# Kernel optimization log

Measured on AMD Instinct MI355X. Metric: run time of the kernel, lower is better.

## Reference

```python
import jax, jax.numpy as jnp
import numpy as np

EMBED_DIM = 768
NUM_HEADS = 12
HEAD_DIM = EMBED_DIM // NUM_HEADS  # 64
SEGMENT_LENGTHS = (2048, 4096, 8192)
DILATION_RATES = (1, 2, 4)
LN_EPS = 1e-5


def setup_inputs() -> dict:
    key = jax.random.key(0)
    ks = jax.random.split(key, 8)
    B, N, E = 2, 8192, EMBED_DIM
    std = 1.0 / np.sqrt(E)
    return {
        "query": jax.random.normal(ks[0], (B, N, E), jnp.float32),
        "key": jax.random.normal(ks[1], (B, N, E), jnp.float32),
        "value": jax.random.normal(ks[2], (B, N, E), jnp.float32),
        "Wqkv": jax.random.normal(ks[3], (3 * E, E), jnp.float32) * std,
        "bqkv": jnp.zeros((3 * E,), jnp.float32),
        "Wo": jax.random.normal(ks[4], (E, E), jnp.float32) * std,
        "bo": jnp.zeros((E,), jnp.float32),
        "ln_w": jnp.ones((E,), jnp.float32),
        "ln_b": jnp.zeros((E,), jnp.float32),
        "is_causal": 0,
    }


def _dilated_attention(q, k, v, is_causal):
    # q, k, v: (b, n, h, d). Heads are partitioned into len(SEGMENT_LENGTHS) groups.
    b, n, h, d = q.shape
    ng = len(SEGMENT_LENGTHS)
    g = h // ng  # heads per group
    scale = 1.0 / np.sqrt(d)
    outs = []
    for i, (s, r) in enumerate(zip(SEGMENT_LENGTHS, DILATION_RATES)):
        off = i % r
        hs = slice(i * g, (i + 1) * g)
        m = n // s          # number of segments
        t = (s - off + r - 1) // r  # dilated tokens per segment
        # (b, m, s, g, d) -> dilated subsample -> (b, m, t, g, d)
        qi = q[:, :, hs].reshape(b, m, s, g, d)[:, :, off::r] * scale
        ki = k[:, :, hs].reshape(b, m, s, g, d)[:, :, off::r]
        vi = v[:, :, hs].reshape(b, m, s, g, d)[:, :, off::r]
        # attention within each segment over the dilated tokens
        scores = jnp.einsum("bmqhd,bmkhd->bmhqk", qi, ki)  # (b,m,g,t,t)
        if is_causal:
            mask = jnp.tril(jnp.ones((t, t), bool))
            scores = jnp.where(mask, scores, jnp.finfo(scores.dtype).min)
        attn = jax.nn.softmax(scores, axis=-1)
        xi = jnp.einsum("bmhqk,bmkhd->bmqhd", attn, vi)  # (b,m,t,g,d)
        # scatter back into full segment positions (zeros elsewhere)
        full = jnp.zeros((b, m, s, g, d), xi.dtype).at[:, :, off::r].set(xi)
        outs.append(full.reshape(b, n, g, d))
    return jnp.concatenate(outs, axis=2)  # (b, n, h, d)


def reference(query, key, value, Wqkv, bqkv, Wo, bo, ln_w, ln_b, is_causal):
    b, n, e = query.shape
    h, d = NUM_HEADS, HEAD_DIM
    q = (query @ Wqkv[:e].T + bqkv[:e]).reshape(b, n, h, d)
    k = (key @ Wqkv[e:2 * e].T + bqkv[e:2 * e]).reshape(b, n, h, d)
    v = (value @ Wqkv[2 * e:].T + bqkv[2 * e:]).reshape(b, n, h, d)
    x = _dilated_attention(q, k, v, is_causal).reshape(b, n, e)
    # LayerNorm
    mu = jnp.mean(x, axis=-1, keepdims=True)
    var = jnp.mean(jnp.square(x - mu), axis=-1, keepdims=True)
    x = (x - mu) * jax.lax.rsqrt(var + LN_EPS) * ln_w + ln_b
    return x @ Wo.T + bo
```

## Files before the change

### kernel.cpp

```cpp
#include <hip/hip_runtime.h>
#include <stdint.h>
#include <stddef.h>

typedef __bf16 bf16;
typedef __attribute__((ext_vector_type(4))) float f32x4;
typedef __attribute__((ext_vector_type(16))) float f32x16;
typedef __attribute__((ext_vector_type(8))) bf16 bf16x8;
typedef __attribute__((ext_vector_type(4))) bf16 bf16x4;

#define INST_STRIDE (2048 * 64)

static __device__ __forceinline__ f32x4 mfma16(bf16x8 a, bf16x8 b, f32x4 c) {
  return __builtin_amdgcn_mfma_f32_16x16x32_bf16(a, b, c, 0, 0, 0);
}
static __device__ __forceinline__ f32x16 mfma32(bf16x8 a, bf16x8 b, f32x16 c) {
  return __builtin_amdgcn_mfma_f32_32x32x16_bf16(a, b, c, 0, 0, 0);
}
static __device__ __forceinline__ void gload16(const void* g, void* l) {
  __builtin_amdgcn_global_load_lds(
      (const __attribute__((address_space(1))) void*)g,
      (__attribute__((address_space(3))) void*)l, 16, 0, 0);
}

__global__ void convert_w(const float* __restrict__ Wqkv, const float* __restrict__ Wo,
                          bf16* __restrict__ wq, bf16* __restrict__ wo) {
  int idx = blockIdx.x * 256 + threadIdx.x;
  const int NQ = 3 * 768 * 768 / 4;
  const float4* src;
  bf16* dst;
  int i;
  if (idx < NQ) { src = (const float4*)Wqkv; dst = wq; i = idx; }
  else          { src = (const float4*)Wo;   dst = wo; i = idx - NQ; }
  float4 v = src[i];
  bf16x4 o = { (bf16)v.x, (bf16)v.y, (bf16)v.z, (bf16)v.w };
  *(bf16x4*)(dst + (size_t)i * 4) = o;
}

__launch_bounds__(256, 4)
__global__ void qkv_gemm(const float* __restrict__ Xq, const float* __restrict__ Xk,
                         const float* __restrict__ Xv, const bf16* __restrict__ Wb,
                         const float* __restrict__ bqkv, bf16* __restrict__ qg,
                         bf16* __restrict__ kg, bf16* __restrict__ vtg) {
  __shared__ __align__(16) bf16 lA[128 * 64];
  __shared__ __align__(16) bf16 lB[128 * 64];
  const int z = blockIdx.z;
  const float* __restrict__ X = (z == 0) ? Xq : ((z == 1) ? Xk : Xv);
  const int bx = blockIdx.x;
  const int nt = blockIdx.y;
  int g, mt;
  if (bx < 128)      { g = 0; mt = bx; }
  else if (bx < 192) { g = 1; mt = bx - 128; }
  else               { g = 2; mt = bx - 192; }
  const int gshift = 13 - g;
  const int gpbm = (8192 >> g) - 1;
  const int ibase = (g == 2) ? 24 : (g << 4);
  const int nseg = 4 >> g;

  const int tid = threadIdx.x;
  const int lane = tid & 63, w = tid >> 6;
  const int wr = w >> 1, wc = w & 1;
  const int l15 = lane & 15, lg = lane >> 4;

  auto maprow = [&](int G) -> size_t {
    int bb = G >> gshift;
    int loc = G & gpbm;
    int seg = loc >> 11, tq = loc & 2047;
    int token = (seg << (11 + g)) + g + (tq << g);
    return (size_t)(bb * 8192 + token);
  };

  const int c8 = tid & 7;
  size_t arow[4];
  int rr[4];
#pragma unroll
  for (int i = 0; i < 4; ++i) {
    rr[i] = (i * 256 + tid) >> 3;
    arow[i] = maprow(mt * 128 + rr[i]);
  }
  const bf16* bsrc[4];
#pragma unroll
  for (int jj = 0; jj < 4; ++jj) {
    int region = w * 4 + jj;
    int row = region * 8 + (lane >> 3);
    int cb = lane & 7;
    bsrc[jj] = Wb + (size_t)(z * 768 + g * 256 + nt * 128 + row) * 768 + ((cb ^ (row & 7)) << 3);
  }

  f32x4 acc[4][4];
#pragma unroll
  for (int i = 0; i < 4; ++i)
#pragma unroll
    for (int j = 0; j < 4; ++j) acc[i][j] = (f32x4){0.f, 0.f, 0.f, 0.f};

  for (int t = 0; t < 12; ++t) {
    const int k0 = t * 64;
#pragma unroll
    for (int jj = 0; jj < 4; ++jj) {
      int region = w * 4 + jj;
      gload16(bsrc[jj] + k0, (char*)lB + region * 1024);
    }
#pragma unroll
    for (int i = 0; i < 4; ++i) {
      const float* src = X + arow[i] * 768 + k0 + c8 * 8;
      float4 v0 = ((const float4*)src)[0];
      float4 v1 = ((const float4*)src)[1];
      bf16x8 o = { (bf16)v0.x, (bf16)v0.y, (bf16)v0.z, (bf16)v0.w,
                   (bf16)v1.x, (bf16)v1.y, (bf16)v1.z, (bf16)v1.w };
      *(bf16x8*)((char*)lA + rr[i] * 128 + ((c8 ^ (rr[i] & 7)) << 4)) = o;
    }
    __syncthreads();
#pragma unroll
    for (int ks = 0; ks < 2; ++ks) {
      bf16x8 af[4], bfr[4];
#pragma unroll
      for (int i = 0; i < 4; ++i) {
        int row = wr * 64 + i * 16 + l15;
        af[i] = *(const bf16x8*)((const char*)lA + row * 128 + (((ks * 4 + lg) ^ (row & 7)) << 4));
        int col = wc * 64 + i * 16 + l15;
        bfr[i] = *(const bf16x8*)((const char*)lB + col * 128 + (((ks * 4 + lg) ^ (col & 7)) << 4));
      }
      __builtin_amdgcn_s_setprio(1);
#pragma unroll
      for (int i = 0; i < 4; ++i)
#pragma unroll
        for (int j = 0; j < 4; ++j) acc[i][j] = mfma16(af[i], bfr[j], acc[i][j]);
      __builtin_amdgcn_s_setprio(0);
    }
    __syncthreads();
  }
#pragma unroll
  for (int j = 0; j < 4; ++j) {
    int gcol = nt * 128 + wc * 64 + j * 16 + l15;
    float bias = bqkv[z * 768 + g * 256 + gcol];
    int hg = gcol >> 6, d = gcol & 63;
    int ho = ibase + hg * nseg;
#pragma unroll
    for (int i = 0; i < 4; ++i) {
      int G0 = mt * 128 + wr * 64 + i * 16 + (lg << 2);
#pragma unroll
      for (int reg = 0; reg < 4; ++reg) {
        int G = G0 + reg;
        int bb = G >> gshift;
        int loc = G & gpbm;
        int seg = loc >> 11, tq = loc & 2047;
        size_t io = (size_t)(bb * 28 + ho + seg) * INST_STRIDE;
        float v = acc[i][j][reg] + bias;
        if (z == 0) {
          qg[io + tq * 64 + d] = (bf16)(v * 0.125f);
        } else if (z == 1) {
          int dsw = (d & 7) | (((d >> 3) ^ (tq & 7)) << 3);
          kg[io + tq * 64 + dsw] = (bf16)v;
        } else {
          int tsw = (tq & ~63) | ((((tq >> 3) & 7) ^ (d & 7)) << 3) | (tq & 7);
          vtg[io + d * 2048 + tsw] = (bf16)v;
        }
      }
    }
  }
}

#define CVTPK(lo_, hi_, out_) \
  asm("v_cvt_pk_bf16_f32 %0, %1, %2" : "=v"(out_) : "v"(lo_), "v"(hi_))

#define MAKE_PA(sv, kb2, dst)                                              \
  do {                                                                     \
    float p0 = __expf(sv[kb2 * 8 + 0] - m);                                \
    float p1 = __expf(sv[kb2 * 8 + 1] - m);                                \
    float p2 = __expf(sv[kb2 * 8 + 2] - m);                                \
    float p3 = __expf(sv[kb2 * 8 + 3] - m);                                \
    float p4 = __expf(sv[kb2 * 8 + 4] - m);                                \
    float p5 = __expf(sv[kb2 * 8 + 5] - m);                                \
    float p6 = __expf(sv[kb2 * 8 + 6] - m);                                \
    float p7 = __expf(sv[kb2 * 8 + 7] - m);                                \
    rs += (p0 + p1) + (p2 + p3) + ((p4 + p5) + (p6 + p7));                 \
    uint32_t a0, a1, a2, a3;                                               \
    CVTPK(p0, p1, a0); CVTPK(p2, p3, a1);                                  \
    CVTPK(p4, p5, a2); CVTPK(p6, p7, a3);                                  \
    asm("v_permlane32_swap_b32 %0, %1" : "+v"(a0), "+v"(a2));              \
    asm("v_permlane32_swap_b32 %0, %1" : "+v"(a1), "+v"(a3));              \
    union { uint32_t u[4]; bf16x8 v; } pk_;                                \
    pk_.u[0] = a0; pk_.u[1] = a1; pk_.u[2] = a2; pk_.u[3] = a3;            \
    dst = pk_.v;                                                           \
  } while (0)

__launch_bounds__(256, 2)
__global__ void attn(const bf16* __restrict__ qg, const bf16* __restrict__ kg,
                     const bf16* __restrict__ vtg, bf16* __restrict__ og,
                     const int* __restrict__ causal_p) {
  __shared__ __align__(16) bf16 lK[2][64 * 64];
  __shared__ __align__(16) bf16 lV[2][64 * 64];
  __shared__ float lSc[4][32];
  const int L = blockIdx.x + (blockIdx.y << 4);
  const int inst = (L & 7) * 7 + ((L >> 3) >> 4);
  const int qt = (L >> 3) & 15;
  const int tid = threadIdx.x, lane = tid & 63, w = tid >> 6;
  const int l31 = lane & 31, hi = lane >> 5;
  const int causal = causal_p[0];
  const size_t ib = (size_t)inst * INST_STRIDE;
  const int qbase = qt * 128 + w * 32;

  bf16x8 qf[4];
#pragma unroll
  for (int dt4 = 0; dt4 < 4; ++dt4)
    qf[dt4] = *(const bf16x8*)(qg + ib + (size_t)(qbase + l31) * 64 + dt4 * 16 + hi * 8);

  f32x16 oacc0 = {0}, oacc1 = {0};
  float m = -1e30f, l = 0.f;

#define STAGE_AT(buf, kt_)                                                       \
  do {                                                                           \
    _Pragma("unroll") for (int j = 0; j < 2; ++j) {                              \
      int region = w * 2 + j;                                                    \
      int r = region * 8 + (lane >> 3);                                          \
      int cb = lane & 7;                                                         \
      gload16(kg + ib + (size_t)((kt_) + r) * 64 + cb * 8,                       \
              (char*)lK[buf] + region * 1024);                                   \
      gload16(vtg + ib + (size_t)r * 2048 + (kt_) + cb * 8,                      \
              (char*)lV[buf] + region * 1024);                                   \
    }                                                                            \
  } while (0)

  STAGE_AT(0, 0);
  __syncthreads();
  int cur = 0;
  for (int kt = 0; kt < 2048; kt += 64) {
    if (kt + 64 < 2048) STAGE_AT(cur ^ 1, kt + 64);
    const bf16* K = lK[cur];
    const bf16* V = lV[cur];
    f32x16 st0 = {0}, st1 = {0};
    __builtin_amdgcn_s_setprio(1);
#pragma unroll
    for (int dt4 = 0; dt4 < 4; ++dt4) {
      int row0 = l31, row1 = 32 + l31;
      bf16x8 kf0 = *(const bf16x8*)((const char*)K + row0 * 128 + (((dt4 * 2 + hi) ^ (row0 & 7)) << 4));
      bf16x8 kf1 = *(const bf16x8*)((const char*)K + row1 * 128 + (((dt4 * 2 + hi) ^ (row1 & 7)) << 4));
      st0 = mfma32(kf0, qf[dt4], st0);
      st1 = mfma32(kf1, qf[dt4], st1);
    }
    __builtin_amdgcn_s_setprio(0);
    if (causal) {
      int q = qbase + l31;
#pragma unroll
      for (int r = 0; r < 16; ++r) {
        int kl = (r & 3) + 8 * (r >> 2) + 4 * hi;
        if (kt + kl > q) st0[r] = -1e30f;
        if (kt + 32 + kl > q) st1[r] = -1e30f;
      }
    }
    float pmax = st0[0];
#pragma unroll
    for (int r = 1; r < 16; ++r) pmax = fmaxf(pmax, st0[r]);
#pragma unroll
    for (int r = 0; r < 16; ++r) pmax = fmaxf(pmax, st1[r]);
    pmax = fmaxf(pmax, __shfl_xor(pmax, 32));
    if (!__all(pmax - m <= 8.f)) {
      float mnew = fmaxf(m, pmax);
      float scale = __expf(m - mnew);
      l *= scale;
      if (!hi) lSc[w][l31] = scale;
      asm volatile("s_waitcnt lgkmcnt(0)" ::: "memory");
      __builtin_amdgcn_sched_barrier(0);
#pragma unroll
      for (int r = 0; r < 16; ++r) {
        float sc = lSc[w][(r & 3) + 8 * (r >> 2) + 4 * hi];
        oacc0[r] *= sc;
        oacc1[r] *= sc;
      }
      m = mnew;
    }
    float rs = 0.f;
    bf16x8 pa0, pa1, pa2, pa3;
    MAKE_PA(st0, 0, pa0);
    MAKE_PA(st0, 1, pa1);
    MAKE_PA(st1, 0, pa2);
    MAKE_PA(st1, 1, pa3);
    rs += __shfl_xor(rs, 32);
    l += rs;
    __builtin_amdgcn_s_setprio(1);
#pragma unroll
    for (int kb = 0; kb < 4; ++kb) {
      bf16x8 pak = (kb == 0) ? pa0 : (kb == 1) ? pa1 : (kb == 2) ? pa2 : pa3;
      int r0 = l31, r1 = 32 + l31;
      bf16x8 vf0 = *(const bf16x8*)((const char*)V + r0 * 128 + (((kb * 2 + hi) ^ (r0 & 7)) << 4));
      bf16x8 vf1 = *(const bf16x8*)((const char*)V + r1 * 128 + (((kb * 2 + hi) ^ (r1 & 7)) << 4));
      oacc0 = mfma32(pak, vf0, oacc0);
      oacc1 = mfma32(pak, vf1, oacc1);
    }
    __builtin_amdgcn_s_setprio(0);
    __syncthreads();
    cur ^= 1;
  }
  if (!hi) lSc[w][l31] = 1.f / l;
  asm volatile("s_waitcnt lgkmcnt(0)" ::: "memory");
  __builtin_amdgcn_sched_barrier(0);
#pragma unroll
  for (int r = 0; r < 16; ++r) {
    int ql = (r & 3) + 8 * (r >> 2) + 4 * hi;
    float linv = lSc[w][ql];
    int q = qbase + ql;
    og[ib + (size_t)q * 64 + l31] = (bf16)(oacc0[r] * linv);
    og[ib + (size_t)q * 64 + 32 + l31] = (bf16)(oacc1[r] * linv);
  }
}

__global__ void ln_gather(const bf16* __restrict__ og, const float* __restrict__ lnw,
                          const float* __restrict__ lnb, bf16* __restrict__ xnorm) {
  const int tok = blockIdx.x * 4 + (threadIdx.x >> 6);
  const int lane = threadIdx.x & 63;
  const int bb = tok >> 13, n = tok & 8191;
  float vals[12];
#pragma unroll
  for (int h = 0; h < 12; ++h) {
    const int grp = h >> 2, hg = h & 3;
    const int sl = 11 + grp;
    int pos = n & ((1 << sl) - 1), seg = n >> sl;
    int rel = pos - grp;
    float v = 0.f;
    if (rel >= 0 && (rel & ((1 << grp) - 1)) == 0) {
      int tq = rel >> grp;
      int base = (grp == 2) ? 24 : (grp << 4);
      size_t inst = (size_t)(bb * 28 + base + hg * (4 >> grp) + seg);
      v = (float)og[inst * INST_STRIDE + (size_t)tq * 64 + lane];
    }
    vals[h] = v;
  }
  float sum = 0.f, sq = 0.f;
#pragma unroll
  for (int h = 0; h < 12; ++h) { sum += vals[h]; sq += vals[h] * vals[h]; }
#pragma unroll
  for (int mm = 32; mm; mm >>= 1) { sum += __shfl_xor(sum, mm); sq += __shfl_xor(sq, mm); }
  const float mu = sum * (1.f / 768.f);
  const float var = sq * (1.f / 768.f) - mu * mu;
  const float rstd = rsqrtf(var + 1e-5f);
  const int tok7 = tok & 7;
#pragma unroll
  for (int h = 0; h < 12; ++h) {
    int e = h * 64 + lane;
    float xn = (vals[h] - mu) * rstd * lnw[e] + lnb[e];
    int esw = h * 64 + ((((lane >> 3) ^ tok7) << 3) | (lane & 7));
    xnorm[(size_t)tok * 768 + esw] = (bf16)xn;
  }
}

__launch_bounds__(512, 2)
__global__ void out_gemm(const bf16* __restrict__ xn, const bf16* __restrict__ wo,
                         const float* __restrict__ bo, float* __restrict__ out) {
  __shared__ __align__(16) bf16 lA[128 * 64];
  __shared__ __align__(16) bf16 lB[256 * 64];
  const int mt = blockIdx.x, nt = blockIdx.y;
  const int tid = threadIdx.x, lane = tid & 63, w = tid >> 6;
  const int wr = w >> 2, wc = w & 3;
  const int l15 = lane & 15, lg = lane >> 4;
  f32x4 acc[4][4];
#pragma unroll
  for (int i = 0; i < 4; ++i)
#pragma unroll
    for (int j = 0; j < 4; ++j) acc[i][j] = (f32x4){0.f, 0.f, 0.f, 0.f};

  for (int k0 = 0; k0 < 768; k0 += 64) {
#pragma unroll
    for (int j = 0; j < 2; ++j) {
      int region = w * 2 + j;
      int r = region * 8 + (lane >> 3);
      int cb = lane & 7;
      gload16(xn + (size_t)(mt * 128 + r) * 768 + k0 + cb * 8, (char*)lA + region * 1024);
    }
#pragma unroll
    for (int j = 0; j < 4; ++j) {
      int region = w * 4 + j;
      int r = region * 8 + (lane >> 3);
      int cb = lane & 7;
      gload16(wo + (size_t)(nt * 256 + r) * 768 + k0 + ((cb ^ (r & 7)) << 3), (char*)lB + region * 1024);
    }
    __syncthreads();
#pragma unroll
    for (int ks = 0; ks < 2; ++ks) {
      bf16x8 af[4], bfr[4];
#pragma unroll
      for (int i = 0; i < 4; ++i) {
        int row = wr * 64 + i * 16 + l15;
        af[i] = *(const bf16x8*)((const char*)lA + row * 128 + (((ks * 4 + lg) ^ (row & 7)) << 4));
        int col = wc * 64 + i * 16 + l15;
        bfr[i] = *(const bf16x8*)((const char*)lB + col * 128 + (((ks * 4 + lg) ^ (col & 7)) << 4));
      }
      __builtin_amdgcn_s_setprio(1);
#pragma unroll
      for (int i = 0; i < 4; ++i)
#pragma unroll
        for (int j = 0; j < 4; ++j) acc[i][j] = mfma16(af[i], bfr[j], acc[i][j]);
      __builtin_amdgcn_s_setprio(0);
    }
    __syncthreads();
  }
#pragma unroll
  for (int j = 0; j < 4; ++j) {
    int col = nt * 256 + wc * 64 + j * 16 + l15;
    float bias = bo[col];
#pragma unroll
    for (int i = 0; i < 4; ++i) {
      int row0 = mt * 128 + wr * 64 + i * 16 + (lg << 2);
#pragma unroll
      for (int reg = 0; reg < 4; ++reg)
        out[(size_t)(row0 + reg) * 768 + col] = acc[i][j][reg] + bias;
    }
  }
}

extern "C" void kernel_launch(void* const* d_in, const int* in_sizes, int n_in,
                              void* d_out, int out_size, void* d_ws, size_t ws_size,
                              hipStream_t stream) {
  (void)in_sizes; (void)n_in; (void)out_size; (void)ws_size;
  const float* query = (const float*)d_in[0];
  const float* key_  = (const float*)d_in[1];
  const float* value = (const float*)d_in[2];
  const float* Wqkv  = (const float*)d_in[3];
  const float* bqkv  = (const float*)d_in[4];
  const float* Wo    = (const float*)d_in[5];
  const float* bo    = (const float*)d_in[6];
  const float* lnw   = (const float*)d_in[7];
  const float* lnb   = (const float*)d_in[8];
  const int* flag    = (const int*)d_in[9];
  float* out = (float*)d_out;

  char* ws = (char*)d_ws;
  size_t off = 0;
  auto alloc = [&](size_t bytes) -> char* {
    char* p = ws + off;
    off += (bytes + 255) & ~(size_t)255;
    return p;
  };
  bf16* wq_bf  = (bf16*)alloc((size_t)3 * 768 * 768 * 2);
  bf16* wo_bf  = (bf16*)alloc((size_t)768 * 768 * 2);
  bf16* qg     = (bf16*)alloc((size_t)56 * INST_STRIDE * 2);
  bf16* kg     = (bf16*)alloc((size_t)56 * INST_STRIDE * 2);
  bf16* vtg    = (bf16*)alloc((size_t)56 * INST_STRIDE * 2);
  bf16* og     = (bf16*)alloc((size_t)56 * INST_STRIDE * 2);
  bf16* xnorm  = (bf16*)alloc((size_t)16384 * 768 * 2);

  convert_w<<<dim3(2304), dim3(256), 0, stream>>>(Wqkv, Wo, wq_bf, wo_bf);
  qkv_gemm<<<dim3(224, 2, 3), dim3(256), 0, stream>>>(query, key_, value, wq_bf, bqkv, qg, kg, vtg);
  attn<<<dim3(16, 56), dim3(256), 0, stream>>>(qg, kg, vtg, og, flag);
  ln_gather<<<dim3(4096), dim3(256), 0, stream>>>(og, lnw, lnb, xnorm);
  out_gemm<<<dim3(128, 3), dim3(512), 0, stream>>>(xnorm, wo_bf, bo, out);
}
```

Before: 246.5 us.

## Pre-convert activations to bf16 and widen QKV GEMM tile to full group width

Adds a separate conversion kernel that turns the fp32 query/key/value tensors into bf16 once, so the QKV GEMM can stage its A tiles with direct global-to-LDS loads instead of register loads plus conversion. The GEMM block grows to 512 threads computing 128x256 tiles, covering the whole group width in a single block. Previously each A tile was read and converted twice across the two N tiles. The cost is an extra pass that writes and re-reads about 75MB of bf16. The workspace buffers for the attention output and the normalised activations now alias the conversion buffer.

```diff
diff --git a/kernel.cpp b/kernel.cpp
--- a/kernel.cpp
+++ b/kernel.cpp
@@ -36,17 +36,31 @@
   *(bf16x4*)(dst + (size_t)i * 4) = o;
 }
 
-__launch_bounds__(256, 4)
-__global__ void qkv_gemm(const float* __restrict__ Xq, const float* __restrict__ Xk,
-                         const float* __restrict__ Xv, const bf16* __restrict__ Wb,
+__global__ void convert_x(const float* __restrict__ Xq, const float* __restrict__ Xk,
+                          const float* __restrict__ Xv, bf16* __restrict__ xbf) {
+  const int idx = blockIdx.x * 256 + threadIdx.x;
+  const int PER = 16384 * 96;
+  const float* src;
+  int c;
+  if (idx < PER)            { src = Xq; c = idx; }
+  else if (idx < 2 * PER)   { src = Xk; c = idx - PER; }
+  else                      { src = Xv; c = idx - 2 * PER; }
+  const float4* s = (const float4*)src + (size_t)c * 2;
+  float4 a = s[0], b = s[1];
+  bf16x8 o = { (bf16)a.x, (bf16)a.y, (bf16)a.z, (bf16)a.w,
+               (bf16)b.x, (bf16)b.y, (bf16)b.z, (bf16)b.w };
+  *(bf16x8*)(xbf + (size_t)idx * 8) = o;
+}
+
+__launch_bounds__(512, 2)
+__global__ void qkv_gemm(const bf16* __restrict__ xbf, const bf16* __restrict__ Wb,
                          const float* __restrict__ bqkv, bf16* __restrict__ qg,
                          bf16* __restrict__ kg, bf16* __restrict__ vtg) {
   __shared__ __align__(16) bf16 lA[128 * 64];
-  __shared__ __align__(16) bf16 lB[128 * 64];
+  __shared__ __align__(16) bf16 lB[256 * 64];
   const int z = blockIdx.z;
-  const float* __restrict__ X = (z == 0) ? Xq : ((z == 1) ? Xk : Xv);
+  const bf16* __restrict__ X = xbf + (size_t)z * 16384 * 768;
   const int bx = blockIdx.x;
-  const int nt = blockIdx.y;
   int g, mt;
   if (bx < 128)      { g = 0; mt = bx; }
   else if (bx < 192) { g = 1; mt = bx - 128; }
@@ -58,7 +72,7 @@
 
   const int tid = threadIdx.x;
   const int lane = tid & 63, w = tid >> 6;
-  const int wr = w >> 1, wc = w & 1;
+  const int wr = w >> 2, wc = w & 3;
   const int l15 = lane & 15, lg = lane >> 4;
 
   auto maprow = [&](int G) -> size_t {
@@ -69,13 +83,13 @@
     return (size_t)(bb * 8192 + token);
   };
 
-  const int c8 = tid & 7;
-  size_t arow[4];
-  int rr[4];
-#pragma unroll
-  for (int i = 0; i < 4; ++i) {
-    rr[i] = (i * 256 + tid) >> 3;
-    arow[i] = maprow(mt * 128 + rr[i]);
+  const bf16* asrc[2];
+#pragma unroll
+  for (int jj = 0; jj < 2; ++jj) {
+    int region = w * 2 + jj;
+    int r = region * 8 + (lane >> 3);
+    int cb = lane & 7;
+    asrc[jj] = X + maprow(mt * 128 + r) * 768 + ((cb ^ (r & 7)) << 3);
   }
   const bf16* bsrc[4];
 #pragma unroll
@@ -83,7 +97,7 @@
     int region = w * 4 + jj;
     int row = region * 8 + (lane >> 3);
     int cb = lane & 7;
-    bsrc[jj] = Wb + (size_t)(z * 768 + g * 256 + nt * 128 + row) * 768 + ((cb ^ (row & 7)) << 3);
+    bsrc[jj] = Wb + (size_t)(z * 768 + g * 256 + row) * 768 + ((cb ^ (row & 7)) << 3);
   }
 
   f32x4 acc[4][4];
@@ -95,19 +109,11 @@
   for (int t = 0; t < 12; ++t) {
     const int k0 = t * 64;
 #pragma unroll
-    for (int jj = 0; jj < 4; ++jj) {
-      int region = w * 4 + jj;
-      gload16(bsrc[jj] + k0, (char*)lB + region * 1024);
-    }
-#pragma unroll
-    for (int i = 0; i < 4; ++i) {
-      const float* src = X + arow[i] * 768 + k0 + c8 * 8;
-      float4 v0 = ((const float4*)src)[0];
-      float4 v1 = ((const float4*)src)[1];
-      bf16x8 o = { (bf16)v0.x, (bf16)v0.y, (bf16)v0.z, (bf16)v0.w,
-                   (bf16)v1.x, (bf16)v1.y, (bf16)v1.z, (bf16)v1.w };
-      *(bf16x8*)((char*)lA + rr[i] * 128 + ((c8 ^ (rr[i] & 7)) << 4)) = o;
-    }
+    for (int jj = 0; jj < 2; ++jj)
+      gload16(asrc[jj] + k0, (char*)lA + (w * 2 + jj) * 1024);
+#pragma unroll
+    for (int jj = 0; jj < 4; ++jj)
+      gload16(bsrc[jj] + k0, (char*)lB + (w * 4 + jj) * 1024);
     __syncthreads();
 #pragma unroll
     for (int ks = 0; ks < 2; ++ks) {
@@ -130,7 +136,7 @@
   }
 #pragma unroll
   for (int j = 0; j < 4; ++j) {
-    int gcol = nt * 128 + wc * 64 + j * 16 + l15;
+    int gcol = wc * 64 + j * 16 + l15;
     float bias = bqkv[z * 768 + g * 256 + gcol];
     int hg = gcol >> 6, d = gcol & 63;
     int ho = ibase + hg * nseg;
@@ -434,11 +440,13 @@
   bf16* qg     = (bf16*)alloc((size_t)56 * INST_STRIDE * 2);
   bf16* kg     = (bf16*)alloc((size_t)56 * INST_STRIDE * 2);
   bf16* vtg    = (bf16*)alloc((size_t)56 * INST_STRIDE * 2);
-  bf16* og     = (bf16*)alloc((size_t)56 * INST_STRIDE * 2);
-  bf16* xnorm  = (bf16*)alloc((size_t)16384 * 768 * 2);
+  bf16* xbf    = (bf16*)alloc((size_t)3 * 16384 * 768 * 2);
+  bf16* og     = xbf;
+  bf16* xnorm  = xbf + (size_t)56 * INST_STRIDE;
 
   convert_w<<<dim3(2304), dim3(256), 0, stream>>>(Wqkv, Wo, wq_bf, wo_bf);
-  qkv_gemm<<<dim3(224, 2, 3), dim3(256), 0, stream>>>(query, key_, value, wq_bf, bqkv, qg, kg, vtg);
+  convert_x<<<dim3(18432), dim3(256), 0, stream>>>(query, key_, value, xbf);
+  qkv_gemm<<<dim3(224, 1, 3), dim3(512), 0, stream>>>(xbf, wq_bf, bqkv, qg, kg, vtg);
   attn<<<dim3(16, 56), dim3(256), 0, stream>>>(qg, kg, vtg, og, flag);
   ln_gather<<<dim3(4096), dim3(256), 0, stream>>>(og, lnw, lnb, xnorm);
   out_gemm<<<dim3(128, 3), dim3(512), 0, stream>>>(xnorm, wo_bf, bo, out);
```

Measured after the change: 259.9 us. 5.4% more time.
